# Performance work log

Hardware: AMD Instinct MI355X
Metric: run time of the kernel (lower is better)

Reference implementation:

```python
import jax, jax.numpy as jnp
import numpy as np
from jax import lax

DN = ('NCHW', 'OIHW', 'NCHW')

def conv(x, w, stride=1):
    return lax.conv_general_dilated(x, w, (stride, stride), 'SAME', dimension_numbers=DN)

def setup_inputs() -> dict:
    key = jax.random.key(0)
    ks = jax.random.split(key, 8)
    B, Cin, H, W = 16, 3, 512, 512
    Cenc, Cdec, n_heads, n_classes = 64, 64, 5, 1
    s = lambda *shape: 0.05
    return {
        'x': jax.random.normal(ks[0], (B, Cin, H, W), jnp.float32),
        'cls_id': jax.random.randint(ks[1], (B,), 0, n_heads, jnp.int32),
        'enc_w': jax.random.normal(ks[2], (Cenc, Cin, 3, 3), jnp.float32) * 0.1,
        'enc_b': jax.random.normal(ks[3], (Cenc,), jnp.float32) * 0.1,
        'dec_w': jax.random.normal(ks[4], (Cdec, Cenc, 3, 3), jnp.float32) * 0.05,
        'dec_b': jax.random.normal(ks[5], (Cdec,), jnp.float32) * 0.1,
        'head_w': jax.random.normal(ks[6], (n_heads, n_classes, Cdec, 3, 3), jnp.float32) * 0.05,
        'head_b': jax.random.normal(ks[7], (n_heads, n_classes), jnp.float32) * 0.1,
    }

def reference(x, cls_id, enc_w, enc_b, dec_w, dec_b, head_w, head_b):
    # encoder: stride-2 conv + relu -> features  [B, Cenc, H/2, W/2]
    f = jax.nn.relu(conv(x, enc_w, 2) + enc_b[None, :, None, None])
    # decoder: 3x3 conv + relu -> decoder_output [B, Cdec, H/2, W/2]
    d = jax.nn.relu(conv(f, dec_w, 1) + dec_b[None, :, None, None])
    # routing: apply segmentation_head[cls_id[b]] to sample b.
    # (gather-by-id -> per-head conv -> backsort) == per-sample gathered-kernel conv
    wk = head_w[cls_id]  # [B, n_classes, Cdec, 3, 3]
    bk = head_b[cls_id]  # [B, n_classes]
    def one_sample(di, wi):  # di: [Cdec,Hd,Wd], wi: [n_classes,Cdec,3,3]
        return conv(di[None], wi, 1)[0]
    masks = jax.vmap(one_sample)(d, wk) + bk[:, :, None, None]
    return masks  # [B, n_classes, H/2, W/2]
```

## Files before the change

### kernel.cpp

```cpp
#include <hip/hip_runtime.h>
#include <stdint.h>

#define NIMG 16
#define HIN 512
#define WIN 512
#define HO 256
#define WO 256
#define HP 258
#define WP 258

typedef unsigned short bf16_t;
typedef unsigned int u32;
typedef short bf16x8 __attribute__((ext_vector_type(8)));
typedef float f32x4 __attribute__((ext_vector_type(4)));
typedef float f32x16 __attribute__((ext_vector_type(16)));

static __device__ __forceinline__ bf16_t f2bf(float f) {
    u32 u = __float_as_uint(f);
    u += 0x7FFFu + ((u >> 16) & 1u);
    return (bf16_t)(u >> 16);
}
static __device__ __forceinline__ float bf_lo(u32 u) { return __uint_as_float(u << 16); }
static __device__ __forceinline__ float bf_hi(u32 u) { return __uint_as_float(u & 0xFFFF0000u); }
static __device__ __forceinline__ u32 pack2(float a, float b) {
    return (u32)f2bf(a) | ((u32)f2bf(b) << 16);
}

__global__ void repack_w(const float* __restrict__ dec_w, const float* __restrict__ enc_w,
                         bf16_t* __restrict__ wB, bf16_t* __restrict__ wEB) {
    int i = blockIdx.x * 256 + threadIdx.x;
    if (i < 36864) {
        int j  = i & 7;
        int l  = (i >> 3) & 63;
        int q  = (i >> 9) & 1;
        int kc = (i >> 10) & 3;
        int r  = i >> 12;
        int co = q * 32 + (l & 31);
        int ci = kc * 16 + ((l >> 5) & 1) * 8 + j;
        wB[i] = f2bf(dec_w[(co * 64 + ci) * 9 + r]);
    } else if (i < 36864 + 2048) {
        int t = i - 36864;
        int j = t & 7;
        int l = (t >> 3) & 63;
        int n = (t >> 9) & 1;
        int s = (t >> 10) & 1;
        int co = n * 32 + (l & 31);
        int k  = s * 16 + ((l >> 5) & 1) * 8 + j;
        wEB[t] = (k < 27) ? f2bf(enc_w[co * 27 + k]) : (bf16_t)0;
    }
}

__global__ void zero_halo(bf16_t* __restrict__ buf, int nimg) {
    const int per_img = 1028 * 8;
    int i = blockIdx.x * 256 + threadIdx.x;
    if (i >= nimg * per_img) return;
    int z = i / per_img;
    int rem = i - z * per_img;
    int p = rem >> 3, q = rem & 7;
    int row, col;
    if (p < 258)      { row = 0;           col = p; }
    else if (p < 516) { row = 257;         col = p - 258; }
    else if (p < 772) { row = p - 516 + 1; col = 0; }
    else              { row = p - 772 + 1; col = 257; }
    *(uint4*)(buf + ((size_t)z * HP * WP + (size_t)row * WP + col) * 64 + q * 8) =
        make_uint4(0u, 0u, 0u, 0u);
}

__global__ __launch_bounds__(512) void encoder_mfma(
    const float* __restrict__ x, const bf16_t* __restrict__ wEB,
    const float* __restrict__ enc_b, bf16_t* __restrict__ f, int b0)
{
    __shared__ __align__(16) bf16_t xt[3][33][34];
    __shared__ __align__(16) bf16_t ot[256 * 72];

    const int tid = threadIdx.x;
    const int w   = tid >> 6;
    const int l   = tid & 63;
    const int z   = blockIdx.z;
    const int b   = b0 + z;
    const int Y0  = blockIdx.y << 5;
    const int X0  = blockIdx.x << 5;

    const int col = l & 31;
    const float bias0 = enc_b[col];
    const float bias1 = enc_b[32 + col];

    const bf16x8* wv = (const bf16x8*)wEB;
    bf16x8 Bf[2][2];
    #pragma unroll
    for (int s = 0; s < 2; ++s) {
        Bf[s][0] = wv[((s * 2 + 0) << 6) + l];
        Bf[s][1] = wv[((s * 2 + 1) << 6) + l];
    }

    const float* xb = x + (size_t)b * 3 * HIN * WIN;
    for (int i = tid; i < 3267; i += 512) {
        int ci  = i / 1089;
        int rem = i - ci * 1089;
        int yy  = rem / 33, xx = rem - yy * 33;
        int iy = Y0 + yy, ix = X0 + xx;
        float v = (iy < HIN && ix < WIN)
                ? xb[(size_t)ci * HIN * WIN + (size_t)iy * WIN + ix] : 0.f;
        xt[ci][yy][xx] = f2bf(v);
    }
    __syncthreads();

    const int row = l & 31;
    const int py  = 2 * w + (row >> 4);
    const int px  = row & 15;
    const int kh  = (l >> 5) * 8;
    bf16x8 A[2];
    #pragma unroll
    for (int s = 0; s < 2; ++s) {
        #pragma unroll
        for (int j = 0; j < 8; ++j) {
            int k = s * 16 + kh + j;
            k = k < 27 ? k : 26;
            int ci  = (k * 29) >> 8;
            int tap = k - ci * 9;
            int dy  = (tap * 11) >> 5;
            int dx  = tap - dy * 3;
            A[s][j] = (short)xt[ci][2 * py + dy][2 * px + dx];
        }
    }

    f32x16 acc[2];
    acc[0] = (f32x16){0.f,0.f,0.f,0.f,0.f,0.f,0.f,0.f,0.f,0.f,0.f,0.f,0.f,0.f,0.f,0.f};
    acc[1] = acc[0];
    acc[0] = __builtin_amdgcn_mfma_f32_32x32x16_bf16(A[0], Bf[0][0], acc[0], 0, 0, 0);
    acc[1] = __builtin_amdgcn_mfma_f32_32x32x16_bf16(A[0], Bf[0][1], acc[1], 0, 0, 0);
    acc[0] = __builtin_amdgcn_mfma_f32_32x32x16_bf16(A[1], Bf[1][0], acc[0], 0, 0, 0);
    acc[1] = __builtin_amdgcn_mfma_f32_32x32x16_bf16(A[1], Bf[1][1], acc[1], 0, 0, 0);

    #pragma unroll
    for (int q = 0; q < 2; ++q) {
        const float bs = q ? bias1 : bias0;
        #pragma unroll
        for (int v = 0; v < 16; ++v) {
            const int grow = (v & 3) + 8 * (v >> 2) + 4 * (l >> 5);
            const int flat = w * 32 + grow;
            float t = acc[q][v] + bs;
            t = t > 0.f ? t : 0.f;
            ot[flat * 72 + q * 32 + col] = f2bf(t);
        }
    }
    __syncthreads();

    bf16_t* fz = f + (size_t)z * HP * WP * 64;
    const int by = blockIdx.y << 4, bx = blockIdx.x << 4;
    #pragma unroll
    for (int it = 0; it < 16; ++it) {
        int i = it * 512 + tid;
        int p = i >> 5, c = i & 31;
        u32 v = *(const u32*)(ot + p * 72 + c * 2);
        int pyy = p >> 4, pxx = p & 15;
        *((u32*)(fz + ((size_t)(by + pyy + 1) * WP + (bx + pxx + 1)) * 64) + c) = v;
    }
}

__global__ __launch_bounds__(512, 4) void decoder_mfma(
    const bf16_t* __restrict__ f, const bf16_t* __restrict__ wB,
    const float* __restrict__ dec_b, bf16_t* __restrict__ d)
{
    __shared__ __align__(16) bf16_t tile[18 * 18 * 64];

    const int tid = threadIdx.x;
    const int w   = tid >> 6;
    const int l   = tid & 63;
    const int z   = blockIdx.z;
    const int y0  = blockIdx.y << 4, x0 = blockIdx.x << 4;

    const int col = l & 31;
    const float bias0 = dec_b[col];
    const float bias1 = dec_b[32 + col];

    const bf16_t* fbase = f + ((size_t)z * HP * WP + (size_t)y0 * WP + x0) * 64;
    for (int i = tid; i < 2592; i += 512) {
        int p   = i >> 3, qq = i & 7;
        int yy  = p / 18, xx = p - yy * 18;
        uint4 v = *(const uint4*)(fbase + ((size_t)yy * WP + xx) * 64 + qq * 8);
        int byteoff = (p * 128 + qq * 16) ^ ((p & 7) << 4);
        *(uint4*)((char*)tile + byteoff) = v;
    }

    f32x16 acc[2];
    acc[0] = (f32x16){0.f,0.f,0.f,0.f,0.f,0.f,0.f,0.f,0.f,0.f,0.f,0.f,0.f,0.f,0.f,0.f};
    acc[1] = acc[0];

    __syncthreads();

    const bf16x8* wBv = (const bf16x8*)wB;
    const int ty_l = (l >> 4) & 1;
    const int tx_l = l & 15;
    const int kh16 = (l >> 5) << 4;

    #pragma unroll
    for (int r = 0; r < 9; ++r) {
        const int dy = r / 3, dx = r - 3 * (r / 3);
        bf16x8 Bf[4][2];
        #pragma unroll
        for (int kc = 0; kc < 4; ++kc) {
            Bf[kc][0] = wBv[(((r * 4 + kc) << 1) + 0) * 64 + l];
            Bf[kc][1] = wBv[(((r * 4 + kc) << 1) + 1) * 64 + l];
        }
        const int p   = (2 * w + ty_l + dy) * 18 + tx_l + dx;
        const int swz = (p & 7) << 4;
        const int pb  = p * 128 + kh16;
        #pragma unroll
        for (int kc = 0; kc < 4; ++kc) {
            bf16x8 a = *(const bf16x8*)((const char*)tile + ((pb + kc * 32) ^ swz));
            acc[0] = __builtin_amdgcn_mfma_f32_32x32x16_bf16(a, Bf[kc][0], acc[0], 0, 0, 0);
            acc[1] = __builtin_amdgcn_mfma_f32_32x32x16_bf16(a, Bf[kc][1], acc[1], 0, 0, 0);
        }
    }

    __syncthreads();
    bf16_t* ot = tile;
    #pragma unroll
    for (int q = 0; q < 2; ++q) {
        const float bs = q ? bias1 : bias0;
        #pragma unroll
        for (int v = 0; v < 16; ++v) {
            const int grow = (v & 3) + 8 * (v >> 2) + 4 * (l >> 5);
            const int flat = w * 32 + grow;
            float t = acc[q][v] + bs;
            t = t > 0.f ? t : 0.f;
            ot[flat * 72 + q * 32 + col] = f2bf(t);
        }
    }
    __syncthreads();

    bf16_t* dz = d + (size_t)z * HP * WP * 64;
    #pragma unroll
    for (int it = 0; it < 16; ++it) {
        int i = it * 512 + tid;
        int p = i >> 5, c = i & 31;
        u32 v = *(const u32*)(ot + p * 72 + c * 2);
        int py = p >> 4, pxx = p & 15;
        *((u32*)(dz + ((size_t)(y0 + py + 1) * WP + (x0 + pxx + 1)) * 64) + c) = v;
    }
}

__global__ __launch_bounds__(256) void head_kernel(
    const bf16_t* __restrict__ d, const float* __restrict__ head_w,
    const float* __restrict__ head_b, const int* __restrict__ cls_id,
    float* __restrict__ out, int b0)
{
    __shared__ __align__(16) bf16_t tile[18 * 18 * 64];
    __shared__ float hw[9][64];

    const int tid = threadIdx.x;
    const int z   = blockIdx.z;
    const int b   = b0 + z;
    const int y0  = blockIdx.y << 4, x0 = blockIdx.x << 4;
    const int cls = cls_id[b];

    for (int i = tid; i < 576; i += 256) {
        int r = i >> 6, ci = i & 63;
        hw[r][ci] = head_w[((size_t)cls * 64 + ci) * 9 + r];
    }
    const bf16_t* dbase = d + ((size_t)z * HP * WP + (size_t)y0 * WP + x0) * 64;
    for (int i = tid; i < 2592; i += 256) {
        int yy  = i / 144;
        int rem = i - yy * 144;
        int xx  = rem >> 3, q = rem & 7;
        int p   = yy * 18 + xx;
        uint4 v = *(const uint4*)(dbase + ((size_t)yy * WP + xx) * 64 + q * 8);
        int byteoff = (p * 128 + q * 16) ^ ((p & 7) << 4);
        *(uint4*)((char*)tile + byteoff) = v;
    }
    __syncthreads();

    const int py = tid >> 4, px = tid & 15;
    float a0 = 0.f, a1 = 0.f, a2 = 0.f, a3 = 0.f;
    #pragma unroll 1
    for (int r = 0; r < 9; ++r) {
        const int dy = r / 3, dx = r - 3 * (r / 3);
        const int p  = (py + dy) * 18 + px + dx;
        const int swz = (p & 7) << 4;
        const float* wr = &hw[r][0];
        #pragma unroll
        for (int q = 0; q < 8; ++q) {
            uint4 v = *(const uint4*)((const char*)tile + ((p * 128 + q * 16) ^ swz));
            float4 w0 = *(const float4*)(wr + q * 8);
            float4 w1 = *(const float4*)(wr + q * 8 + 4);
            float t0 = fmaf(bf_lo(v.x), w0.x, fmaf(bf_hi(v.x), w0.y, 0.f));
            float t1 = fmaf(bf_lo(v.y), w0.z, fmaf(bf_hi(v.y), w0.w, 0.f));
            float t2 = fmaf(bf_lo(v.z), w1.x, fmaf(bf_hi(v.z), w1.y, 0.f));
            float t3 = fmaf(bf_lo(v.w), w1.z, fmaf(bf_hi(v.w), w1.w, 0.f));
            a0 += t0; a1 += t1; a2 += t2; a3 += t3;
        }
    }
    const float acc = head_b[cls] + (a0 + a1) + (a2 + a3);
    out[(size_t)b * (HO * WO) + (size_t)(y0 + py) * WO + (x0 + px)] = acc;
}

extern "C" void kernel_launch(void* const* d_in, const int* in_sizes, int n_in,
                              void* d_out, int out_size, void* d_ws, size_t ws_size,
                              hipStream_t stream) {
    const float* x      = (const float*)d_in[0];
    const int*   cls_id = (const int*)  d_in[1];
    const float* enc_w  = (const float*)d_in[2];
    const float* enc_b  = (const float*)d_in[3];
    const float* dec_w  = (const float*)d_in[4];
    const float* dec_b  = (const float*)d_in[5];
    const float* head_w = (const float*)d_in[6];
    const float* head_b = (const float*)d_in[7];
    float* out = (float*)d_out;

    const size_t WB_RESERVE = 131072;
    const size_t PER_IMG    = (size_t)HP * WP * 64 * 2;
    char* ws = (char*)d_ws;
    bf16_t* wB  = (bf16_t*)ws;
    bf16_t* wEB = (bf16_t*)(ws + 81920);

    size_t avail = (ws_size > WB_RESERVE) ? (ws_size - WB_RESERVE) : 0;
    int C = (int)(avail / (2 * PER_IMG));
    if (C < 1) C = 1;
    if (C > NIMG) C = NIMG;

    bf16_t* fbuf = (bf16_t*)(ws + WB_RESERVE);
    bf16_t* dbuf = (bf16_t*)(ws + WB_RESERVE + (size_t)C * PER_IMG);

    repack_w<<<dim3(152), 256, 0, stream>>>(dec_w, enc_w, wB, wEB);
    {
        int nthr = C * 1028 * 8;
        int nblk = (nthr + 255) / 256;
        zero_halo<<<dim3(nblk), 256, 0, stream>>>(fbuf, C);
        zero_halo<<<dim3(nblk), 256, 0, stream>>>(dbuf, C);
    }

    int n_rounds = (NIMG + C - 1) / C;
    int per = (NIMG + n_rounds - 1) / n_rounds;
    for (int b0 = 0; b0 < NIMG; b0 += per) {
        const int n = (NIMG - b0 < per) ? (NIMG - b0) : per;
        encoder_mfma<<<dim3(16, 16, n), 512, 0, stream>>>(x, wEB, enc_b, fbuf, b0);
        decoder_mfma<<<dim3(16, 16, n), 512, 0, stream>>>(fbuf, wB, dec_b, dbuf);
        head_kernel <<<dim3(16, 16, n), 256, 0, stream>>>(dbuf, head_w, head_b, cls_id, out, b0);
    }
}
```

Measured before the change: 240.5 us.

## Interleave channel layout so epilogues store directly without LDS staging

Changes the stored channel order of the encoder and decoder outputs to an interleaved layout (channel c and c+32 packed together). Each lane can then write a packed pair of bf16 values straight to global memory, with no LDS transpose or extra barriers. The decoder weights and head weights are permuted to match. This removes the LDS staging and its syncs, and the decoder occupancy hint rises from 4 to 6. The cost is that global stores become 4-byte scattered writes with less coalescing.

```diff
diff --git a/kernel.cpp b/kernel.cpp
--- a/kernel.cpp
+++ b/kernel.cpp
@@ -14,6 +14,7 @@
 typedef short bf16x8 __attribute__((ext_vector_type(8)));
 typedef float f32x4 __attribute__((ext_vector_type(4)));
 typedef float f32x16 __attribute__((ext_vector_type(16)));
+
 
 static __device__ __forceinline__ bf16_t f2bf(float f) {
     u32 u = __float_as_uint(f);
@@ -35,8 +36,9 @@
         int q  = (i >> 9) & 1;
         int kc = (i >> 10) & 3;
         int r  = i >> 12;
-        int co = q * 32 + (l & 31);
-        int ci = kc * 16 + ((l >> 5) & 1) * 8 + j;
+        int co  = q * 32 + (l & 31);
+        int pos = kc * 16 + ((l >> 5) & 1) * 8 + j;
+        int ci  = (pos & 1) * 32 + (pos >> 1);
         wB[i] = f2bf(dec_w[(co * 64 + ci) * 9 + r]);
     } else if (i < 36864 + 2048) {
         int t = i - 36864;
@@ -71,7 +73,6 @@
     const float* __restrict__ enc_b, bf16_t* __restrict__ f, int b0)
 {
     __shared__ __align__(16) bf16_t xt[3][33][34];
-    __shared__ __align__(16) bf16_t ot[256 * 72];
 
     const int tid = threadIdx.x;
     const int w   = tid >> 6;
@@ -132,33 +133,21 @@
     acc[0] = __builtin_amdgcn_mfma_f32_32x32x16_bf16(A[1], Bf[1][0], acc[0], 0, 0, 0);
     acc[1] = __builtin_amdgcn_mfma_f32_32x32x16_bf16(A[1], Bf[1][1], acc[1], 0, 0, 0);
 
-    #pragma unroll
-    for (int q = 0; q < 2; ++q) {
-        const float bs = q ? bias1 : bias0;
-        #pragma unroll
-        for (int v = 0; v < 16; ++v) {
-            const int grow = (v & 3) + 8 * (v >> 2) + 4 * (l >> 5);
-            const int flat = w * 32 + grow;
-            float t = acc[q][v] + bs;
-            t = t > 0.f ? t : 0.f;
-            ot[flat * 72 + q * 32 + col] = f2bf(t);
-        }
-    }
-    __syncthreads();
-
     bf16_t* fz = f + (size_t)z * HP * WP * 64;
     const int by = blockIdx.y << 4, bx = blockIdx.x << 4;
     #pragma unroll
-    for (int it = 0; it < 16; ++it) {
-        int i = it * 512 + tid;
-        int p = i >> 5, c = i & 31;
-        u32 v = *(const u32*)(ot + p * 72 + c * 2);
-        int pyy = p >> 4, pxx = p & 15;
-        *((u32*)(fz + ((size_t)(by + pyy + 1) * WP + (bx + pxx + 1)) * 64) + c) = v;
-    }
-}
-
-__global__ __launch_bounds__(512, 4) void decoder_mfma(
+    for (int v = 0; v < 16; ++v) {
+        const int grow = (v & 3) + 8 * (v >> 2) + 4 * (l >> 5);
+        const int flat = w * 32 + grow;
+        const int pyy = flat >> 4, pxx = flat & 15;
+        float t0 = acc[0][v] + bias0;  t0 = t0 > 0.f ? t0 : 0.f;
+        float t1 = acc[1][v] + bias1;  t1 = t1 > 0.f ? t1 : 0.f;
+        *(u32*)(fz + ((size_t)(by + pyy + 1) * WP + (bx + pxx + 1)) * 64 + 2 * col) =
+            pack2(t0, t1);
+    }
+}
+
+__global__ __launch_bounds__(512, 6) void decoder_mfma(
     const bf16_t* __restrict__ f, const bf16_t* __restrict__ wB,
     const float* __restrict__ dec_b, bf16_t* __restrict__ d)
 {
@@ -214,30 +203,16 @@
         }
     }
 
-    __syncthreads();
-    bf16_t* ot = tile;
-    #pragma unroll
-    for (int q = 0; q < 2; ++q) {
-        const float bs = q ? bias1 : bias0;
-        #pragma unroll
-        for (int v = 0; v < 16; ++v) {
-            const int grow = (v & 3) + 8 * (v >> 2) + 4 * (l >> 5);
-            const int flat = w * 32 + grow;
-            float t = acc[q][v] + bs;
-            t = t > 0.f ? t : 0.f;
-            ot[flat * 72 + q * 32 + col] = f2bf(t);
-        }
-    }
-    __syncthreads();
-
     bf16_t* dz = d + (size_t)z * HP * WP * 64;
     #pragma unroll
-    for (int it = 0; it < 16; ++it) {
-        int i = it * 512 + tid;
-        int p = i >> 5, c = i & 31;
-        u32 v = *(const u32*)(ot + p * 72 + c * 2);
-        int py = p >> 4, pxx = p & 15;
-        *((u32*)(dz + ((size_t)(y0 + py + 1) * WP + (x0 + pxx + 1)) * 64) + c) = v;
+    for (int v = 0; v < 16; ++v) {
+        const int grow = (v & 3) + 8 * (v >> 2) + 4 * (l >> 5);
+        const int flat = w * 32 + grow;
+        const int py = flat >> 4, px = flat & 15;
+        float t0 = acc[0][v] + bias0;  t0 = t0 > 0.f ? t0 : 0.f;
+        float t1 = acc[1][v] + bias1;  t1 = t1 > 0.f ? t1 : 0.f;
+        *(u32*)(dz + ((size_t)(y0 + py + 1) * WP + (x0 + px + 1)) * 64 + 2 * col) =
+            pack2(t0, t1);
     }
 }
 
@@ -256,8 +231,9 @@
     const int cls = cls_id[b];
 
     for (int i = tid; i < 576; i += 256) {
-        int r = i >> 6, ci = i & 63;
-        hw[r][ci] = head_w[((size_t)cls * 64 + ci) * 9 + r];
+        int r = i >> 6, s = i & 63;
+        int ci = (s & 1) * 32 + (s >> 1);
+        hw[r][s] = head_w[((size_t)cls * 64 + ci) * 9 + r];
     }
     const bf16_t* dbase = d + ((size_t)z * HP * WP + (size_t)y0 * WP + x0) * 64;
     for (int i = tid; i < 2592; i += 256) {
```

After: 234.6 us. 1.03x faster.
